# Kernel tuning notes

Hardware: AMD Instinct MI355X
Metric: run time of the kernel (lower is better)

Reference implementation:

```python
import jax, jax.numpy as jnp
import numpy as np

TAU = 0.5
EPS = 1e-8  # torch CosineSimilarity eps


def _normalize(v):
    # matches torch cosine sim: divide by max(||v||, eps)
    n = jnp.linalg.norm(v, axis=-1, keepdims=True)
    return v / jnp.maximum(n, EPS)


def setup_inputs() -> dict:
    key = jax.random.key(0)
    k1, k2 = jax.random.split(key)
    N, D = 4096, 256
    x = jax.random.normal(k1, (N, D), dtype=jnp.float32)
    y = jax.random.normal(k2, (N, D), dtype=jnp.float32)
    return {"x": x, "y": y}


def reference(x, y):
    n = x.shape[0]
    xn = _normalize(x)
    yn = _normalize(y)
    inv_tau = 1.0 / TAU
    sim_xx = (xn @ xn.T) * inv_tau  # [n, n]
    sim_yy = (yn @ yn.T) * inv_tau
    sim_xy = (xn @ yn.T) * inv_tau
    neg_inf = jnp.float32(-jnp.inf)
    diag = jnp.arange(n)
    sim_xx = sim_xx.at[diag, diag].set(neg_inf)
    sim_yy = sim_yy.at[diag, diag].set(neg_inf)
    scores1 = jnp.concatenate([sim_xy, sim_xx], axis=-1)          # [n, 2n]
    scores2 = jnp.concatenate([sim_yy, sim_xy.T], axis=-1)        # [n, 2n]
    scores = jnp.concatenate([scores1, scores2], axis=-2)          # [2n, 2n]
    targets = jnp.arange(2 * n)
    logp = jax.nn.log_softmax(scores, axis=-1)
    loss = -jnp.mean(logp[jnp.arange(2 * n), targets])
    return loss
```

## Files before the change

kernel.cpp:

```cpp
#include <hip/hip_runtime.h>
#include <hip/hip_bf16.h>


#define NROWS 8192
#define DDIM  256
#define BM    256
#define BN    64
#define COLSPLIT 16
#define COLS_PER (NROWS / COLSPLIT)
#define NT (COLS_PER / BN)

typedef __attribute__((ext_vector_type(8))) __bf16 bf16x8_t;
typedef __attribute__((ext_vector_type(4))) float  f32x4_t;

typedef __attribute__((address_space(1))) const void* as1_cvp;
typedef __attribute__((address_space(3))) void*       as3_vp;

#if __has_builtin(__builtin_amdgcn_exp2f)
#define EXP2F __builtin_amdgcn_exp2f
#else
#define EXP2F exp2f
#endif

#define TWO_LOG2E 2.8853900817779268f

__global__ __launch_bounds__(256) void normalize_diag_kernel(
    const float* __restrict__ x, const float* __restrict__ y,
    __hip_bfloat16* __restrict__ zb, float* __restrict__ rowdiag,
    float* __restrict__ rowsum) {
  const int g = blockIdx.x * 256 + threadIdx.x;
  if (g < NROWS) rowsum[g] = 0.f;

  const int w = threadIdx.x >> 6, lane = threadIdx.x & 63;
  const int i = blockIdx.x * 4 + w;
  const float4 xv = ((const float4*)(x + (size_t)i * DDIM))[lane];
  const float4 yv = ((const float4*)(y + (size_t)i * DDIM))[lane];
  float ssx = xv.x * xv.x + xv.y * xv.y + xv.z * xv.z + xv.w * xv.w;
  float ssy = yv.x * yv.x + yv.y * yv.y + yv.z * yv.z + yv.w * yv.w;
  float sxy = xv.x * yv.x + xv.y * yv.y + xv.z * yv.z + xv.w * yv.w;
  #pragma unroll
  for (int off = 32; off > 0; off >>= 1) {
    ssx += __shfl_xor(ssx, off, 64);
    ssy += __shfl_xor(ssy, off, 64);
    sxy += __shfl_xor(sxy, off, 64);
  }
  const float sclx = 1.0f / fmaxf(sqrtf(ssx), 1e-8f);
  const float scly = 1.0f / fmaxf(sqrtf(ssy), 1e-8f);
  __hip_bfloat16 px[4], py[4];
  px[0] = __float2bfloat16(xv.x * sclx); px[1] = __float2bfloat16(xv.y * sclx);
  px[2] = __float2bfloat16(xv.z * sclx); px[3] = __float2bfloat16(xv.w * sclx);
  py[0] = __float2bfloat16(yv.x * scly); py[1] = __float2bfloat16(yv.y * scly);
  py[2] = __float2bfloat16(yv.z * scly); py[3] = __float2bfloat16(yv.w * scly);
  *(short4*)(zb + (size_t)i * DDIM + lane * 4)            = *(short4*)px;
  *(short4*)(zb + (size_t)(i + 4096) * DDIM + lane * 4)   = *(short4*)py;
  if (lane == 0) rowdiag[i] = 2.0f * sxy * sclx * scly;
}

__global__ __launch_bounds__(512) void gram_lse_kernel(
    const __hip_bfloat16* __restrict__ zbh, float* __restrict__ rowsum) {
  __shared__ short smem[2][BN * DDIM];

  const short* zs = (const short*)zbh;
  const char* zbytes = (const char*)zs;
  const int tid  = threadIdx.x;
  const int w    = tid >> 6;
  const int lane = tid & 63;
  const int lhi  = lane >> 4;
  const int llo  = lane & 15;
  const int i0 = (blockIdx.x >> 4) * BM;
  const int c0 = (blockIdx.x & 15) * COLS_PER;
  const bool has_diag = ((blockIdx.x >> 5) == (blockIdx.x & 15));

  const int arow0 = i0 + w * 32 + llo;
  const float TBF = __bfloat162float(__float2bfloat16(TWO_LOG2E));
  bf16x8_t afa[8], afb[8];
  #pragma unroll
  for (int ks = 0; ks < 8; ++ks) {
    afa[ks] = *(const bf16x8_t*)(zs + (size_t)arow0 * DDIM + ks * 32 + lhi * 8);
    afb[ks] = *(const bf16x8_t*)(zs + (size_t)(arow0 + 16) * DDIM + ks * 32 + lhi * 8);
    #pragma unroll
    for (int e = 0; e < 8; ++e) {
      afa[ks][e] = (__bf16)((float)afa[ks][e] * TBF);
      afb[ks][e] = (__bf16)((float)afb[ks][e] * TBF);
    }
  }

  int soff[4], loff[4];
  #pragma unroll
  for (int it = 0; it < 4; ++it) {
    const int o    = it * 8192 + tid * 16;
    const int cr   = o >> 9;
    const int slot = (o >> 4) & 31;
    soff[it] = cr * 512 + ((slot ^ (cr & 31)) << 4);
    loff[it] = it * 8192 + w * 1024;
  }

#define STAGE(buf, ct_) do {                                                  \
    const size_t cbase = (size_t)(c0 + (ct_) * BN) * 512;                     \
    _Pragma("unroll")                                                         \
    for (int it = 0; it < 4; ++it) {                                          \
      __builtin_amdgcn_global_load_lds(                                       \
          (as1_cvp)(zbytes + cbase + (size_t)soff[it]),                       \
          (as3_vp)((char*)smem[buf] + loff[it]), 16, 0, 0);                   \
    }                                                                         \
  } while (0)

  float racc0[4] = {0.f, 0.f, 0.f, 0.f};
  float racc1[4] = {0.f, 0.f, 0.f, 0.f};
  const int gr0 = i0 + w * 32 + lhi * 4;
  const int gr1 = gr0 + 16;

  STAGE(0, 0);
  asm volatile("s_waitcnt vmcnt(0)" ::: "memory");
  __syncthreads();
  int cur = 0;

  for (int ct = 0; ct < NT; ++ct) {
    if (ct + 1 < NT) STAGE(cur ^ 1, ct + 1);
    const int cb = c0 + ct * BN;

    #pragma unroll
    for (int nt = 0; nt < 4; ++nt) {
      const int cr = nt * 16 + llo;
      f32x4_t acc0 = {0.f, 0.f, 0.f, 0.f};
      f32x4_t acc1 = {0.f, 0.f, 0.f, 0.f};
      #pragma unroll
      for (int ks = 0; ks < 8; ++ks) {
        const int kg = ks * 4 + lhi;
        const bf16x8_t bfrag = *(const bf16x8_t*)(
            (const char*)smem[cur] + cr * 512 + ((kg ^ (cr & 31)) << 4));
        acc0 = __builtin_amdgcn_mfma_f32_16x16x32_bf16(afa[ks], bfrag, acc0, 0, 0, 0);
        acc1 = __builtin_amdgcn_mfma_f32_16x16x32_bf16(afb[ks], bfrag, acc1, 0, 0, 0);
      }
      if (has_diag) {
        const int gc = cb + cr;
        #pragma unroll
        for (int j = 0; j < 4; ++j) {
          racc0[j] += ((gr0 + j) != gc) ? EXP2F(acc0[j]) : 0.f;
          racc1[j] += ((gr1 + j) != gc) ? EXP2F(acc1[j]) : 0.f;
        }
      } else {
        #pragma unroll
        for (int j = 0; j < 4; ++j) {
          racc0[j] += EXP2F(acc0[j]);
          racc1[j] += EXP2F(acc1[j]);
        }
      }
    }
    asm volatile("s_waitcnt vmcnt(0)" ::: "memory");
    __syncthreads();
    cur ^= 1;
  }
#undef STAGE

  #pragma unroll
  for (int j = 0; j < 4; ++j) {
    float v0 = racc0[j], v1 = racc1[j];
    v0 += __shfl_xor(v0, 1, 16); v1 += __shfl_xor(v1, 1, 16);
    v0 += __shfl_xor(v0, 2, 16); v1 += __shfl_xor(v1, 2, 16);
    v0 += __shfl_xor(v0, 4, 16); v1 += __shfl_xor(v1, 4, 16);
    v0 += __shfl_xor(v0, 8, 16); v1 += __shfl_xor(v1, 8, 16);
    if (llo == 0) {
      atomicAdd(&rowsum[gr0 + j], v0);
      atomicAdd(&rowsum[gr1 + j], v1);
    }
  }
}

__global__ __launch_bounds__(256) void finalize_kernel(
    const float* __restrict__ rowsum, const float* __restrict__ rowdiag,
    float* __restrict__ out) {
  const int t = threadIdx.x;
  float s = 0.f;
  for (int r4 = t; r4 < NROWS / 4; r4 += 256) {
    const float4 v = ((const float4*)rowsum)[r4];
    s += __logf(v.x) + __logf(v.y) + __logf(v.z) + __logf(v.w);
  }
  for (int i4 = t; i4 < 4096 / 4; i4 += 256) {
    const float4 d = ((const float4*)rowdiag)[i4];
    s -= 2.0f * (d.x + d.y + d.z + d.w);
  }
  #pragma unroll
  for (int off = 32; off > 0; off >>= 1) s += __shfl_xor(s, off, 64);
  __shared__ float wsum[4];
  const int w = t >> 6, lane = t & 63;
  if (lane == 0) wsum[w] = s;
  __syncthreads();
  if (t == 0) out[0] = (wsum[0] + wsum[1] + wsum[2] + wsum[3]) / (float)NROWS;
}

extern "C" void kernel_launch(void* const* d_in, const int* in_sizes, int n_in,
                              void* d_out, int out_size, void* d_ws, size_t ws_size,
                              hipStream_t stream) {
  const float* x = (const float*)d_in[0];
  const float* y = (const float*)d_in[1];
  float* out = (float*)d_out;

  char* ws = (char*)d_ws;
  __hip_bfloat16* zb = (__hip_bfloat16*)ws;
  float* rowsum  = (float*)(ws + (size_t)NROWS * DDIM * 2);
  float* rowdiag = rowsum + NROWS;

  normalize_diag_kernel<<<1024, 256, 0, stream>>>(x, y, zb, rowdiag, rowsum);
  gram_lse_kernel<<<512, 512, 0, stream>>>(zb, rowsum);
  finalize_kernel<<<1, 256, 0, stream>>>(rowsum, rowdiag, out);
}
```

Before: 56.61 us.

## Deepen LDS pipeline to four smaller buffers with interleaved async loads

Halves the column tile to 32 and switches from double buffering to a 4-slot ring with 3 tiles in flight. Async global-to-LDS loads for tile ct+3 are issued inside the MFMA loop, and partial vmcnt waits replace the full drain before each barrier. It also raises wave priority around the MFMA block with s_setprio. The aim is to hide global load latency better, at the cost of twice as many barriers and smaller tiles per synchronisation.

Result: no change. 56.73 us (+0.2%).

```diff
diff --git a/kernel.cpp b/kernel.cpp
--- a/kernel.cpp
+++ b/kernel.cpp
@@ -5,7 +5,7 @@
 #define NROWS 8192
 #define DDIM  256
 #define BM    256
-#define BN    64
+#define BN    32
 #define COLSPLIT 16
 #define COLS_PER (NROWS / COLSPLIT)
 #define NT (COLS_PER / BN)
@@ -58,7 +58,7 @@
 
 __global__ __launch_bounds__(512) void gram_lse_kernel(
     const __hip_bfloat16* __restrict__ zbh, float* __restrict__ rowsum) {
-  __shared__ short smem[2][BN * DDIM];
+  __shared__ short smem[4][BN * DDIM];
 
   const short* zs = (const short*)zbh;
   const char* zbytes = (const char*)zs;
@@ -85,24 +85,21 @@
     }
   }
 
-  int soff[4], loff[4];
-  #pragma unroll
-  for (int it = 0; it < 4; ++it) {
+  int soff[2], loff[2];
+  #pragma unroll
+  for (int it = 0; it < 2; ++it) {
     const int o    = it * 8192 + tid * 16;
     const int cr   = o >> 9;
     const int slot = (o >> 4) & 31;
-    soff[it] = cr * 512 + ((slot ^ (cr & 31)) << 4);
+    soff[it] = cr * 512 + ((slot ^ cr) << 4);
     loff[it] = it * 8192 + w * 1024;
   }
 
-#define STAGE(buf, ct_) do {                                                  \
-    const size_t cbase = (size_t)(c0 + (ct_) * BN) * 512;                     \
-    _Pragma("unroll")                                                         \
-    for (int it = 0; it < 4; ++it) {                                          \
-      __builtin_amdgcn_global_load_lds(                                       \
-          (as1_cvp)(zbytes + cbase + (size_t)soff[it]),                       \
-          (as3_vp)((char*)smem[buf] + loff[it]), 16, 0, 0);                   \
-    }                                                                         \
+#define STAGE1(buf_, ct_, it_) do {                                           \
+    const size_t cbase_ = (size_t)(c0 + (ct_) * BN) * 512;                    \
+    __builtin_amdgcn_global_load_lds(                                         \
+        (as1_cvp)(zbytes + cbase_ + (size_t)soff[it_]),                       \
+        (as3_vp)((char*)smem[buf_] + loff[it_]), 16, 0, 0);                   \
   } while (0)
 
   float racc0[4] = {0.f, 0.f, 0.f, 0.f};
@@ -110,48 +107,55 @@
   const int gr0 = i0 + w * 32 + lhi * 4;
   const int gr1 = gr0 + 16;
 
-  STAGE(0, 0);
-  asm volatile("s_waitcnt vmcnt(0)" ::: "memory");
-  __syncthreads();
-  int cur = 0;
-
-  for (int ct = 0; ct < NT; ++ct) {
-    if (ct + 1 < NT) STAGE(cur ^ 1, ct + 1);
-    const int cb = c0 + ct * BN;
-
-    #pragma unroll
-    for (int nt = 0; nt < 4; ++nt) {
-      const int cr = nt * 16 + llo;
-      f32x4_t acc0 = {0.f, 0.f, 0.f, 0.f};
-      f32x4_t acc1 = {0.f, 0.f, 0.f, 0.f};
-      #pragma unroll
-      for (int ks = 0; ks < 8; ++ks) {
-        const int kg = ks * 4 + lhi;
-        const bf16x8_t bfrag = *(const bf16x8_t*)(
-            (const char*)smem[cur] + cr * 512 + ((kg ^ (cr & 31)) << 4));
-        acc0 = __builtin_amdgcn_mfma_f32_16x16x32_bf16(afa[ks], bfrag, acc0, 0, 0, 0);
-        acc1 = __builtin_amdgcn_mfma_f32_16x16x32_bf16(afb[ks], bfrag, acc1, 0, 0, 0);
-      }
-      if (has_diag) {
-        const int gc = cb + cr;
-        #pragma unroll
-        for (int j = 0; j < 4; ++j) {
-          racc0[j] += ((gr0 + j) != gc) ? EXP2F(acc0[j]) : 0.f;
-          racc1[j] += ((gr1 + j) != gc) ? EXP2F(acc1[j]) : 0.f;
-        }
-      } else {
-        #pragma unroll
-        for (int j = 0; j < 4; ++j) {
-          racc0[j] += EXP2F(acc0[j]);
-          racc1[j] += EXP2F(acc1[j]);
-        }
-      }
-    }
-    asm volatile("s_waitcnt vmcnt(0)" ::: "memory");
-    __syncthreads();
-    cur ^= 1;
-  }
-#undef STAGE
+  #pragma unroll
+  for (int t = 0; t < 3; ++t) {
+    STAGE1(t, t, 0);
+    STAGE1(t, t, 1);
+  }
+
+#define TILE(ct_, VMSTR) do {                                                 \
+    asm volatile("s_waitcnt " VMSTR ::: "memory");                            \
+    __syncthreads();                                                          \
+    const int cb = c0 + (ct_) * BN;                                           \
+    const short* bufp = smem[(ct_) & 3];                                      \
+    _Pragma("unroll")                                                         \
+    for (int nt = 0; nt < 2; ++nt) {                                          \
+      if ((ct_) + 3 < NT) STAGE1(((ct_) + 3) & 3, (ct_) + 3, nt);             \
+      const int cr = nt * 16 + llo;                                           \
+      f32x4_t acc0 = {0.f, 0.f, 0.f, 0.f};                                    \
+      f32x4_t acc1 = {0.f, 0.f, 0.f, 0.f};                                    \
+      __builtin_amdgcn_s_setprio(1);                                          \
+      _Pragma("unroll")                                                       \
+      for (int ks = 0; ks < 8; ++ks) {                                        \
+        const int kg = ks * 4 + lhi;                                          \
+        const bf16x8_t bfrag = *(const bf16x8_t*)(                            \
+            (const char*)bufp + cr * 512 + ((kg ^ cr) << 4));                 \
+        acc0 = __builtin_amdgcn_mfma_f32_16x16x32_bf16(afa[ks], bfrag, acc0, 0, 0, 0); \
+        acc1 = __builtin_amdgcn_mfma_f32_16x16x32_bf16(afb[ks], bfrag, acc1, 0, 0, 0); \
+      }                                                                       \
+      __builtin_amdgcn_s_setprio(0);                                          \
+      if (has_diag) {                                                         \
+        const int gc = cb + cr;                                               \
+        _Pragma("unroll")                                                     \
+        for (int j = 0; j < 4; ++j) {                                         \
+          racc0[j] += ((gr0 + j) != gc) ? EXP2F(acc0[j]) : 0.f;               \
+          racc1[j] += ((gr1 + j) != gc) ? EXP2F(acc1[j]) : 0.f;               \
+        }                                                                     \
+      } else {                                                                \
+        _Pragma("unroll")                                                     \
+        for (int j = 0; j < 4; ++j) {                                         \
+          racc0[j] += EXP2F(acc0[j]);                                         \
+          racc1[j] += EXP2F(acc1[j]);                                         \
+        }                                                                     \
+      }                                                                       \
+    }                                                                         \
+  } while (0)
+
+  for (int ct = 0; ct < NT - 2; ++ct) TILE(ct, "vmcnt(4)");
+  TILE(NT - 2, "vmcnt(2)");
+  TILE(NT - 1, "vmcnt(0)");
+#undef TILE
+#undef STAGE1
 
   #pragma unroll
   for (int j = 0; j < 4; ++j) {
```
